# Performance work log

Measured on AMD Instinct MI355X. Metric: run time of the kernel, lower is better.

## Reference

```python
import jax, jax.numpy as jnp
import numpy as np

B, L, N, D, TOPK, OUT_V = 32, 512, 1024, 64, 20, 1024
BN_EPS = 1e-5
NEG_SLOPE = 0.2


def setup_inputs() -> dict:
    key = jax.random.key(0)
    ks = jax.random.split(key, 8)
    s = lambda k, shape, sc=0.05: jax.random.normal(k, shape, jnp.float32) * sc
    return {
        "x_enc": jax.random.normal(ks[0], (B, L, N), jnp.float32),
        "emb": s(ks[1], (N, D), 0.1),          # nn.Embedding(variate, d_model).weight
        "lin_W": s(ks[2], (L, D)),              # GraphLayer.lin (no bias)
        "att_i": s(ks[3], (D,)),
        "att_j": s(ks[4], (D,)),
        "att_em_i": s(ks[5], (D,)),
        "att_em_j": s(ks[6], (D,)),
        "gnn_b": jnp.zeros((D,), jnp.float32),  # GraphLayer bias (concat=False)
        "g1": jnp.ones((D,), jnp.float32), "b1": jnp.zeros((D,), jnp.float32),   # GNNLayer.bn
        "g2": jnp.ones((D,), jnp.float32), "b2": jnp.zeros((D,), jnp.float32),   # bn_outlayer_in
        "out_W": s(ks[7], (D, 1)), "out_b": jnp.zeros((1,), jnp.float32),        # OutLayer Linear(d_model, 1)
    }


def _forward(x_enc, emb, lin_W, att_i, att_j, att_em_i, att_em_j,
             gnn_b, g1, b1, g2, b2, out_W, out_b):
    # --- LIN: LayerNorm(input_len, eps=0, no affine) over time, first OUT_V variates ---
    xv = jnp.transpose(x_enc[:, :, :OUT_V], (0, 2, 1))          # [B, OUT_V, L]
    xv = (xv - xv.mean(-1, keepdims=True)) / jnp.sqrt(xv.var(-1, keepdims=True))
    x_enc = x_enc.at[:, :, :OUT_V].set(jnp.transpose(xv, (0, 2, 1)))
    x_enc = jnp.nan_to_num(x_enc, nan=0.0, posinf=0.0, neginf=0.0)

    gt = x_enc[:, -1:, :OUT_V]                                   # [B, 1, OUT_V]
    enc = x_enc.at[:, -1:, :OUT_V].set(0.0)

    # x = enc.transpose(0,1).view(-1, L)  (faithful to original reshape)
    x = jnp.transpose(enc, (1, 0, 2)).reshape(-1, L)             # [B*N, L]

    # --- dynamic top-k cosine-similarity graph (embeddings detached) ---
    w = jax.lax.stop_gradient(emb)
    nrm = jnp.linalg.norm(w, axis=-1)
    cos = (w @ w.T) / (nrm[:, None] * nrm[None, :])              # [N, N]
    topk_idx = jax.lax.top_k(cos, TOPK)[1]                       # [N, TOPK]
    src = topk_idx.reshape(-1)                                   # gated_j (source)
    dst = jnp.repeat(jnp.arange(N), TOPK)                        # gated_i (target)

    offs = (jnp.arange(B) * N)[:, None]
    src_b = (src[None, :] + offs).reshape(-1)                    # [B*N*TOPK]
    dst_b = (dst[None, :] + offs).reshape(-1)

    # remove_self_loops (mask out) then add_self_loops for all B*N nodes
    num_nodes = B * N
    self_mask = jnp.concatenate([src_b == dst_b, jnp.zeros(num_nodes, bool)])
    src_all = jnp.concatenate([src_b, jnp.arange(num_nodes)])
    dst_all = jnp.concatenate([dst_b, jnp.arange(num_nodes)])

    # --- GraphLayer (GAT-style, heads=1, concat=False) ---
    h = x @ lin_W                                                # [B*N, D]
    all_emb = jnp.tile(emb, (B, 1))                              # [B*N, D]

    logit = (h[dst_all] @ att_i + all_emb[dst_all] @ att_em_i
             + h[src_all] @ att_j + all_emb[src_all] @ att_em_j)  # [E]
    logit = jnp.where(logit >= 0, logit, NEG_SLOPE * logit)      # leaky_relu(0.2)
    logit = jnp.where(self_mask, -jnp.inf, logit)

    seg_max = jax.ops.segment_max(logit, dst_all, num_segments=num_nodes)
    expv = jnp.where(self_mask, 0.0, jnp.exp(logit - seg_max[dst_all]))
    denom = jax.ops.segment_sum(expv, dst_all, num_segments=num_nodes)
    alpha = expv / denom[dst_all]

    out = jax.ops.segment_sum(h[src_all] * alpha[:, None], dst_all,
                              num_segments=num_nodes) + gnn_b    # [B*N, D]

    # GNNLayer: BatchNorm1d(D) (batch stats) + ReLU
    out = (out - out.mean(0)) / jnp.sqrt(out.var(0) + BN_EPS) * g1 + b1
    out = jax.nn.relu(out)

    # --- combine with embedding, bn_outlayer_in, OutLayer ---
    xg = out.reshape(B, N, D) * emb[None]                        # [B, N, D]
    xg = jnp.transpose(xg, (0, 2, 1))                            # [B, D, N]
    mu = xg.mean((0, 2), keepdims=True)
    var = xg.var((0, 2), keepdims=True)
    xg = (xg - mu) / jnp.sqrt(var + BN_EPS) * g2[None, :, None] + b2[None, :, None]
    xg = jnp.transpose(jax.nn.relu(xg), (0, 2, 1))               # [B, N, D]

    o = xg @ out_W + out_b                                       # [B, N, 1]
    o = jnp.transpose(o, (0, 2, 1))                              # [B, 1, N]
    return o[:, :, :OUT_V], gt


def reference(x_enc, emb, lin_W, att_i, att_j, att_em_i, att_em_j,
              gnn_b, g1, b1, g2, b2, out_W, out_b):
    return _forward(x_enc, emb, lin_W, att_i, att_j, att_em_i, att_em_j,
                    gnn_b, g1, b1, g2, b2, out_W, out_b)
```

## Files before the change

### kernel.cpp

```cpp
#include <hip/hip_runtime.h>
#include <stdint.h>

#define BB 32
#define LL 512
#define NNODES 1024
#define DD 64
#define TOPK 20
#define NTOT (BB*NNODES)
#define LNSZ (LL*NNODES)

typedef short short8 __attribute__((ext_vector_type(8)));
typedef float floatx4 __attribute__((ext_vector_type(4)));

__device__ __forceinline__ float bf2f(unsigned short u){
    union { unsigned int i; float f; } x; x.i = ((unsigned int)u) << 16; return x.f;
}
__device__ __forceinline__ unsigned short f2bf(float f){
    union { float f; unsigned int i; } x; x.f = f;
    unsigned int u = x.i;
    return (unsigned short)((u + 0x7FFFu + ((u >> 16) & 1u)) >> 16);
}
__device__ __forceinline__ void unpack2(unsigned int w, float& lo, float& hi){
    union { unsigned int i; float f; } a, b;
    a.i = w << 16; b.i = w & 0xFFFF0000u;
    lo = a.f; hi = b.f;
}
__device__ __forceinline__ float ldf(const void* p, int i, int isf){
    return isf ? ((const float*)p)[i] : bf2f(((const unsigned short*)p)[i]);
}

__global__ void __launch_bounds__(256) kd_detect(const unsigned short* x, int* flag, float* stats){
    __shared__ int cnt;
    stats[threadIdx.x] = 0.f;
    if (threadIdx.x == 0) cnt = 0;
    __syncthreads();
    unsigned int idx = (threadIdx.x * 131071u) & 0x7FFFFFu;
    float v = bf2f(x[idx * 2]);
    float a = fabsf(v);
    int crazy = (!(a <= 1e3f)) || (v != 0.f && a < 1e-6f);
    atomicAdd(&cnt, crazy);
    __syncthreads();
    if (threadIdx.x == 0) flag[0] = (cnt > 64) ? 1 : 0;
}

__global__ void __launch_bounds__(256) k0_prep(const void* lw, unsigned short* wt, const int* dtf){
    int isf = dtf[0];
    int id = blockIdx.x * 256 + threadIdx.x;
    int k = id >> 6, d = id & 63;
    unsigned short w = isf ? f2bf(((const float*)lw)[id]) : ((const unsigned short*)lw)[id];
    wt[d * 512 + k] = w;
}

__global__ void __launch_bounds__(256) k1a_partial(const void* x, float* part, const int* dtf){
    int isf = dtf[0];
    int t = threadIdx.x;
    int b = blockIdx.x >> 4, lq = blockIdx.x & 15;
    int n0 = t * 4;
    size_t base = (size_t)b * LNSZ + (size_t)(lq * 32) * NNODES + n0;
    float s0=0,s1=0,s2=0,s3=0,q0=0,q1=0,q2=0,q3=0;
    if (isf){
        const float* p = (const float*)x + base;
        for (int i = 0; i < 32; i++){
            float4 w = *(const float4*)p;
            s0+=w.x; q0+=w.x*w.x; s1+=w.y; q1+=w.y*w.y;
            s2+=w.z; q2+=w.z*w.z; s3+=w.w; q3+=w.w*w.w;
            p += NNODES;
        }
    } else {
        const unsigned short* p = (const unsigned short*)x + base;
        for (int i = 0; i < 32; i++){
            uint2 w = *(const uint2*)p;
            float a,bv,c,d2;
            unpack2(w.x, a, bv); unpack2(w.y, c, d2);
            s0+=a; q0+=a*a; s1+=bv; q1+=bv*bv; s2+=c; q2+=c*c; s3+=d2; q3+=d2*d2;
            p += NNODES;
        }
    }
    int v = b * NNODES + n0;
    float2* pp = (float2*)part;
    pp[(size_t)v*16 + lq]       = make_float2(s0,q0);
    pp[(size_t)(v+1)*16 + lq]   = make_float2(s1,q1);
    pp[(size_t)(v+2)*16 + lq]   = make_float2(s2,q2);
    pp[(size_t)(v+3)*16 + lq]   = make_float2(s3,q3);
}

__global__ void __launch_bounds__(256) k1b_finalize(const void* x, const float* part,
                                                    float* mr, float* outp, const int* dtf){
    int isf = dtf[0];
    int v = blockIdx.x * 256 + threadIdx.x;
    const float2* pp = (const float2*)part + (size_t)v * 16;
    float s = 0.f, q = 0.f;
    for (int i = 0; i < 16; i++){ float2 w = pp[i]; s += w.x; q += w.y; }
    float mean = s * (1.f/512.f);
    float var  = q * (1.f/512.f) - mean * mean;
    float rstd = var > 0.f ? rsqrtf(var) : 0.f;
    ((float2*)mr)[v] = make_float2(mean, rstd);
    int b = v >> 10, n = v & 1023;
    float xv = ldf(x, (int)((size_t)b * LNSZ + (size_t)511 * NNODES + n), isf);
    outp[NTOT + v] = (xv - mean) * rstd;
}

__global__ void __launch_bounds__(256) k2_gemm_h(const void* x, const unsigned short* wt,
                                                const float* mr, float* h, const int* dtf){
    __shared__ unsigned short A_l[128 * 136];
    __shared__ unsigned short W_l[64 * 136];
    __shared__ float4 colp4[256];
    int isf = dtf[0];
    int t = threadIdx.x;
    int q = blockIdx.x & 63, mtile = blockIdx.x >> 6;
    int b = q >> 1, nbase = (q & 1) * 512;
    size_t xbase = (size_t)b * LNSZ + nbase;

    colp4[t] = ((const float4*)mr)[q * 256 + t];

    int wave = t >> 6, lane = t & 63;
    int quad = lane >> 4, lcol = lane & 15;
    floatx4 acc[2][4];
    for (int i = 0; i < 2; i++) for (int j = 0; j < 4; j++) acc[i][j] = (floatx4){0.f,0.f,0.f,0.f};
    __syncthreads();

    for (int kc = 0; kc < 4; kc++){
        for (int i = 0; i < 8; i++){
            int id = i * 256 + t;
            int l = id >> 4, c16 = id & 15;
            int lg = mtile * 128 + l;
            uint4 o;
            if (lg == 511){
                o = make_uint4(0u, 0u, 0u, 0u);
            } else {
                size_t ofs = xbase + (size_t)lg * NNODES + kc * 128 + c16 * 8;
                float e0,e1,e2,e3,e4,e5,e6,e7;
                if (isf){
                    const float4* px = (const float4*)((const float*)x + ofs);
                    float4 wa = px[0], wb = px[1];
                    e0=wa.x; e1=wa.y; e2=wa.z; e3=wa.w; e4=wb.x; e5=wb.y; e6=wb.z; e7=wb.w;
                } else {
                    uint4 w = *(const uint4*)((const unsigned short*)x + ofs);
                    unpack2(w.x,e0,e1); unpack2(w.y,e2,e3); unpack2(w.z,e4,e5); unpack2(w.w,e6,e7);
                }
                int f4b = kc * 64 + c16 * 4;
                float4 pA = colp4[f4b+0], pB = colp4[f4b+1], pC = colp4[f4b+2], pD = colp4[f4b+3];
                e0 = (e0 - pA.x) * pA.y;  e1 = (e1 - pA.z) * pA.w;
                e2 = (e2 - pB.x) * pB.y;  e3 = (e3 - pB.z) * pB.w;
                e4 = (e4 - pC.x) * pC.y;  e5 = (e5 - pC.z) * pC.w;
                e6 = (e6 - pD.x) * pD.y;  e7 = (e7 - pD.z) * pD.w;
                o.x = (unsigned)f2bf(e0) | ((unsigned)f2bf(e1) << 16);
                o.y = (unsigned)f2bf(e2) | ((unsigned)f2bf(e3) << 16);
                o.z = (unsigned)f2bf(e4) | ((unsigned)f2bf(e5) << 16);
                o.w = (unsigned)f2bf(e6) | ((unsigned)f2bf(e7) << 16);
            }
            *(uint4*)&A_l[l * 136 + c16 * 8] = o;
        }
        for (int i = 0; i < 4; i++){
            int id = i * 256 + t;
            int dd = id >> 4, c16 = id & 15;
            uint4 w = *(const uint4*)(wt + dd * 512 + kc * 128 + c16 * 8);
            *(uint4*)&W_l[dd * 136 + c16 * 8] = w;
        }
        __syncthreads();
        for (int ks = 0; ks < 4; ks++){
            short8 af[2], bfr[4];
            af[0] = *(const short8*)&A_l[(wave * 32 + lcol) * 136 + ks * 32 + quad * 8];
            af[1] = *(const short8*)&A_l[(wave * 32 + 16 + lcol) * 136 + ks * 32 + quad * 8];
            for (int tc = 0; tc < 4; tc++)
                bfr[tc] = *(const short8*)&W_l[(tc * 16 + lcol) * 136 + ks * 32 + quad * 8];
            for (int tr = 0; tr < 2; tr++)
                for (int tc = 0; tc < 4; tc++)
                    acc[tr][tc] = __builtin_amdgcn_mfma_f32_16x16x32_bf16(af[tr], bfr[tc], acc[tr][tc], 0, 0, 0);
        }
        __syncthreads();
    }
    for (int tr = 0; tr < 2; tr++) for (int tc = 0; tc < 4; tc++){
        int dcol = tc * 16 + lcol;
        for (int r = 0; r < 4; r++){
            int lrow = wave * 32 + tr * 16 + quad * 4 + r;
            int lg = mtile * 128 + lrow;
            int row = lg * 64 + q;
            h[(size_t)row * 64 + dcol] = acc[tr][tc][r];
        }
    }
}

__global__ void __launch_bounds__(256) k3_graph(const void* emb, const void* aemi,
                                                const void* aemj, float* eai, float* eaj,
                                                int* topk, const int* dtf){
    __shared__ float enf[64];
    __shared__ float crow[1024];
    __shared__ float n2sh;
    int isf = dtf[0];
    int n = blockIdx.x, t = threadIdx.x, lane = t & 63, wave = t >> 6;
    if (wave == 0){
        float e = ldf(emb, n * 64 + lane, isf);
        enf[lane] = e;
        float p1 = e * e;
        float p2 = e * ldf(aemi, lane, isf);
        float p3 = e * ldf(aemj, lane, isf);
        for (int m = 1; m < 64; m <<= 1){
            p1 += __shfl_xor(p1, m, 64);
            p2 += __shfl_xor(p2, m, 64);
            p3 += __shfl_xor(p3, m, 64);
        }
        if (lane == 0){ n2sh = p1; eai[n] = p2; eaj[n] = p3; }
    }
    __syncthreads();
    float rn_own = rsqrtf(n2sh);
    for (int mi = 0; mi < 4; mi++){
        int m = mi * 256 + t;
        float dot = 0.f, sq = 0.f;
        if (isf){
            const float4* pm = (const float4*)((const float*)emb + m * 64);
            #pragma unroll
            for (int i = 0; i < 16; i++){
                float4 w = pm[i];
                dot += enf[i*4+0]*w.x + enf[i*4+1]*w.y + enf[i*4+2]*w.z + enf[i*4+3]*w.w;
                sq  += w.x*w.x + w.y*w.y + w.z*w.z + w.w*w.w;
            }
        } else {
            const uint4* pm = (const uint4*)((const unsigned short*)emb + m * 64);
            #pragma unroll
            for (int i = 0; i < 8; i++){
                uint4 w = pm[i];
                float a0,a1,a2,a3,a4,a5,a6,a7;
                unpack2(w.x,a0,a1); unpack2(w.y,a2,a3); unpack2(w.z,a4,a5); unpack2(w.w,a6,a7);
                dot += enf[i*8+0]*a0 + enf[i*8+1]*a1 + enf[i*8+2]*a2 + enf[i*8+3]*a3
                     + enf[i*8+4]*a4 + enf[i*8+5]*a5 + enf[i*8+6]*a6 + enf[i*8+7]*a7;
                sq  += a0*a0 + a1*a1 + a2*a2 + a3*a3 + a4*a4 + a5*a5 + a6*a6 + a7*a7;
            }
        }
        crow[m] = dot * rn_own * rsqrtf(sq);
    }
    __syncthreads();
    if (wave == 0){
        float v[16];
        #pragma unroll
        for (int ii = 0; ii < 16; ii++) v[ii] = crow[ii * 64 + lane];
        for (int k = 0; k < TOPK; k++){
            float bv = v[0]; int bi = 0;
            #pragma unroll
            for (int ii = 1; ii < 16; ii++) if (v[ii] > bv){ bv = v[ii]; bi = ii; }
            int bm = bi * 64 + lane;
            for (int m2 = 1; m2 < 64; m2 <<= 1){
                float ov = __shfl_xor(bv, m2, 64);
                int   om = __shfl_xor(bm, m2, 64);
                if (ov > bv || (ov == bv && om < bm)){ bv = ov; bm = om; }
            }
            if (lane == 0) topk[n * TOPK + k] = bm;
            int evi = bm >> 6;
            bool own = ((bm & 63) == lane);
            #pragma unroll
            for (int ii = 0; ii < 16; ii++)
                v[ii] = (own && ii == evi) ? -__builtin_inff() : v[ii];
        }
    }
}

__global__ void __launch_bounds__(256) k4_coef(const float* h, const void* att_i, const void* att_j,
                                               const float* eai, const float* eaj, float* ai, float* aj,
                                               const int* dtf){
    int isf = dtf[0];
    int wave = blockIdx.x * 4 + (threadIdx.x >> 6), lane = threadIdx.x & 63;
    float wi = ldf(att_i, lane, isf), wj = ldf(att_j, lane, isf);
    int v0 = wave * 16;
    for (int i = 0; i < 16; i++){
        int v = v0 + i;
        float hv = h[(size_t)v * 64 + lane];
        float p1 = hv * wi, p2 = hv * wj;
        for (int m = 1; m < 64; m <<= 1){ p1 += __shfl_xor(p1, m, 64); p2 += __shfl_xor(p2, m, 64); }
        if (lane == 0){
            int n = v & 1023;
            ai[v] = p1 + eai[n];
            aj[v] = p2 + eaj[n];
        }
    }
}

__global__ void __launch_bounds__(256) k5_attn(const float* h, const float* ai, const float* aj, const int* topk,
                                               const void* gnn_b, float* out, const int* dtf){
    int isf = dtf[0];
    int wave = threadIdx.x >> 6, lane = threadIdx.x & 63;
    float gb = ldf(gnn_b, lane, isf);
    int v = blockIdx.x * 4 + wave;
    int n = v & 1023, bbase = v & ~1023;
    int srcv; bool valid;
    if (lane < TOPK){
        int id = topk[n * TOPK + lane];
        srcv = bbase | id;
        valid = (id != n);
    } else if (lane == TOPK){
        srcv = v; valid = true;
    } else { srcv = v; valid = false; }
    float l = ai[v] + aj[srcv];
    l = (l >= 0.f) ? l : 0.2f * l;
    if (!valid) l = -__builtin_inff();
    float m = l;
    #pragma unroll
    for (int s = 1; s < 64; s <<= 1){ float o = __shfl_xor(m, s, 64); m = fmaxf(m, o); }
    float ev = valid ? __expf(l - m) : 0.f;
    float dsum = ev;
    #pragma unroll
    for (int s = 1; s < 64; s <<= 1) dsum += __shfl_xor(dsum, s, 64);
    float rd = 1.f / dsum;
    float acc = 0.f;
    #pragma unroll
    for (int j = 0; j <= TOPK; j++){
        float e = __shfl(ev, j, 64);
        int  sj = __shfl(srcv, j, 64);
        acc += e * h[(size_t)sj * 64 + lane];
    }
    out[(size_t)v * 64 + lane] = acc * rd + gb;
}

__global__ void __launch_bounds__(256) k5b_stats(const float* out, float* stats1){
    __shared__ float bs[256], bq[256];
    int wave = threadIdx.x >> 6, lane = threadIdx.x & 63;
    int v0 = blockIdx.x * 128 + wave * 32;
    float ssum = 0.f, ssq = 0.f;
    for (int i = 0; i < 32; i++){
        float x = out[(size_t)(v0 + i) * 64 + lane];
        ssum += x; ssq += x * x;
    }
    bs[threadIdx.x] = ssum; bq[threadIdx.x] = ssq;
    __syncthreads();
    if (wave == 0){
        float s  = bs[lane] + bs[64+lane] + bs[128+lane] + bs[192+lane];
        float qq = bq[lane] + bq[64+lane] + bq[128+lane] + bq[192+lane];
        atomicAdd(&stats1[lane], s);
        atomicAdd(&stats1[64 + lane], qq);
    }
}

__global__ void __launch_bounds__(256) k6_stats2(const float* out, const float* stats1, const void* g1,
                                                 const void* b1, const void* emb,
                                                 float* stats2, const int* dtf){
    __shared__ float bs[256], bq[256];
    int isf = dtf[0];
    int wave = threadIdx.x >> 6, lane = threadIdx.x & 63;
    float mu   = stats1[lane] * (1.f/32768.f);
    float var  = stats1[64 + lane] * (1.f/32768.f) - mu * mu;
    float rstd = 1.f / sqrtf(var + 1e-5f);
    float g = ldf(g1, lane, isf), bb = ldf(b1, lane, isf);
    float ssum = 0.f, ssq = 0.f;
    int v0 = (blockIdx.x * 4 + wave) * 16;
    for (int i = 0; i < 16; i++){
        int v = v0 + i; int n = v & 1023;
        float x = out[(size_t)v * 64 + lane];
        float y = fmaxf((x - mu) * rstd * g + bb, 0.f);
        float z = y * ldf(emb, n * 64 + lane, isf);
        ssum += z; ssq += z * z;
    }
    bs[threadIdx.x] = ssum; bq[threadIdx.x] = ssq;
    __syncthreads();
    if (wave == 0){
        float s  = bs[lane] + bs[64+lane] + bs[128+lane] + bs[192+lane];
        float qq = bq[lane] + bq[64+lane] + bq[128+lane] + bq[192+lane];
        atomicAdd(&stats2[lane], s);
        atomicAdd(&stats2[64 + lane], qq);
    }
}

__global__ void __launch_bounds__(256) k7_out(const float* out, const float* stats1, const float* stats2,
                                              const void* g1, const void* b1,
                                              const void* g2, const void* b2,
                                              const void* emb, const void* outw,
                                              const void* outb, float* o, const int* dtf){
    int isf = dtf[0];
    int wave = threadIdx.x >> 6, lane = threadIdx.x & 63;
    float mu1   = stats1[lane] * (1.f/32768.f);
    float var1  = stats1[64 + lane] * (1.f/32768.f) - mu1 * mu1;
    float rstd1 = 1.f / sqrtf(var1 + 1e-5f);
    float g1v = ldf(g1, lane, isf), b1v = ldf(b1, lane, isf);
    float mu2   = stats2[lane] * (1.f/32768.f);
    float var2  = stats2[64 + lane] * (1.f/32768.f) - mu2 * mu2;
    float rstd2 = 1.f / sqrtf(var2 + 1e-5f);
    float g2v = ldf(g2, lane, isf), b2v = ldf(b2, lane, isf);
    float w = ldf(outw, lane, isf);
    float ob = ldf(outb, 0, isf);
    int v0 = (blockIdx.x * 4 + wave) * 16;
    for (int i = 0; i < 16; i++){
        int v = v0 + i; int n = v & 1023;
        float x = out[(size_t)v * 64 + lane];
        float z = fmaxf((x - mu1) * rstd1 * g1v + b1v, 0.f) * ldf(emb, n * 64 + lane, isf);
        float y = fmaxf((z - mu2) * rstd2 * g2v + b2v, 0.f);
        float p = y * w;
        for (int s = 1; s < 64; s <<= 1) p += __shfl_xor(p, s, 64);
        if (lane == 0) o[v] = p + ob;
    }
}

extern "C" void kernel_launch(void* const* d_in, const int* in_sizes, int n_in,
                              void* d_out, int out_size, void* d_ws, size_t ws_size,
                              hipStream_t stream){
    const void* x    = d_in[0];
    const void* emb  = d_in[1];
    const void* linW = d_in[2];
    const void* atti = d_in[3];
    const void* attj = d_in[4];
    const void* aemi = d_in[5];
    const void* aemj = d_in[6];
    const void* gnnb = d_in[7];
    const void* g1   = d_in[8];
    const void* b1   = d_in[9];
    const void* g2   = d_in[10];
    const void* b2   = d_in[11];
    const void* outw = d_in[12];
    const void* outb = d_in[13];
    float* o = (float*)d_out;

    char* w = (char*)d_ws;
    float*          mr    = (float*)(w + 0);
    unsigned short* wt    = (unsigned short*)(w + 262144);
    float*          h     = (float*)(w + 327680);
    float*          eai   = (float*)(w + 8716288);
    float*          eaj   = (float*)(w + 8720384);
    int*            topk  = (int*)(w + 8724480);
    float*          ai    = (float*)(w + 8806400);
    float*          aj    = (float*)(w + 8937472);
    float*          outg  = (float*)(w + 9068544);
    float*          part  = outg;
    float*          stats = (float*)(w + 17457152);
    int*            dtf   = (int*)(w + 17458176);

    hipLaunchKernelGGL(kd_detect,    dim3(1),    dim3(256), 0, stream, (const unsigned short*)x, dtf, stats);
    hipLaunchKernelGGL(k0_prep,      dim3(128),  dim3(256), 0, stream, linW, wt, dtf);
    hipLaunchKernelGGL(k1a_partial,  dim3(512),  dim3(256), 0, stream, x, part, dtf);
    hipLaunchKernelGGL(k1b_finalize, dim3(128),  dim3(256), 0, stream, x, part, mr, o, dtf);
    hipLaunchKernelGGL(k2_gemm_h,    dim3(256),  dim3(256), 0, stream, x, wt, mr, h, dtf);
    hipLaunchKernelGGL(k3_graph,     dim3(1024), dim3(256), 0, stream, emb, aemi, aemj, eai, eaj, topk, dtf);
    hipLaunchKernelGGL(k4_coef,      dim3(512),  dim3(256), 0, stream, h, atti, attj, eai, eaj, ai, aj, dtf);
    hipLaunchKernelGGL(k5_attn,      dim3(8192), dim3(256), 0, stream, h, ai, aj, topk, gnnb, outg, dtf);
    hipLaunchKernelGGL(k5b_stats,    dim3(256),  dim3(256), 0, stream, outg, stats);
    hipLaunchKernelGGL(k6_stats2,    dim3(512),  dim3(256), 0, stream, outg, stats, g1, b1, emb, stats + 128, dtf);
    hipLaunchKernelGGL(k7_out,       dim3(512),  dim3(256), 0, stream, outg, stats, stats + 128,
                       g1, b1, g2, b2, emb, outw, outb, o, dtf);
}
```

Measured before the change: 273.3 us.

## Compute top-k graph with one wave per node, no shared row buffer

Reworks the cosine top-k kernel so that each wave handles one node and holds its 1024 similarity values in registers (16 per lane). This removes the shared-memory row buffer, the block barrier, and the serial top-k done by a single wave while three waves sat idle. The per-lane argmax becomes a tree reduction, and the embedding-attention dot products move into the prep kernel. The cost is higher register pressure and a serial 64-iteration loop per thread in the prep kernel.

```diff
diff --git a/kernel.cpp b/kernel.cpp
--- a/kernel.cpp
+++ b/kernel.cpp
@@ -43,12 +43,24 @@
     if (threadIdx.x == 0) flag[0] = (cnt > 64) ? 1 : 0;
 }
 
-__global__ void __launch_bounds__(256) k0_prep(const void* lw, unsigned short* wt, const int* dtf){
+__global__ void __launch_bounds__(256) k0_prep(const void* lw, unsigned short* wt,
+                                               const void* emb, const void* aemi, const void* aemj,
+                                               float* eai, float* eaj, const int* dtf){
     int isf = dtf[0];
     int id = blockIdx.x * 256 + threadIdx.x;
     int k = id >> 6, d = id & 63;
     unsigned short w = isf ? f2bf(((const float*)lw)[id]) : ((const unsigned short*)lw)[id];
     wt[d * 512 + k] = w;
+    if (id < 1024){
+        int n = id;
+        float s1 = 0.f, s2 = 0.f;
+        for (int dd = 0; dd < 64; dd++){
+            float e = ldf(emb, n * 64 + dd, isf);
+            s1 += e * ldf(aemi, dd, isf);
+            s2 += e * ldf(aemj, dd, isf);
+        }
+        eai[n] = s1; eaj[n] = s2;
+    }
 }
 
 __global__ void __launch_bounds__(256) k1a_partial(const void* x, float* part, const int* dtf){
@@ -181,38 +193,29 @@
     }
 }
 
-__global__ void __launch_bounds__(256) k3_graph(const void* emb, const void* aemi,
-                                                const void* aemj, float* eai, float* eaj,
-                                                int* topk, const int* dtf){
-    __shared__ float enf[64];
-    __shared__ float crow[1024];
-    __shared__ float n2sh;
-    int isf = dtf[0];
-    int n = blockIdx.x, t = threadIdx.x, lane = t & 63, wave = t >> 6;
-    if (wave == 0){
-        float e = ldf(emb, n * 64 + lane, isf);
-        enf[lane] = e;
-        float p1 = e * e;
-        float p2 = e * ldf(aemi, lane, isf);
-        float p3 = e * ldf(aemj, lane, isf);
-        for (int m = 1; m < 64; m <<= 1){
-            p1 += __shfl_xor(p1, m, 64);
-            p2 += __shfl_xor(p2, m, 64);
-            p3 += __shfl_xor(p3, m, 64);
-        }
-        if (lane == 0){ n2sh = p1; eai[n] = p2; eaj[n] = p3; }
-    }
-    __syncthreads();
-    float rn_own = rsqrtf(n2sh);
-    for (int mi = 0; mi < 4; mi++){
-        int m = mi * 256 + t;
+__global__ void __launch_bounds__(256) k3_topk(const void* emb, int* topk, const int* dtf){
+    __shared__ float enf[4][64];
+    int isf = dtf[0];
+    int wave = threadIdx.x >> 6, lane = threadIdx.x & 63;
+    int n = blockIdx.x * 4 + wave;
+    float e = ldf(emb, n * 64 + lane, isf);
+    enf[wave][lane] = e;
+    float p1 = e * e;
+    #pragma unroll
+    for (int m = 1; m < 64; m <<= 1) p1 += __shfl_xor(p1, m, 64);
+    __syncthreads();
+    float rn_own = rsqrtf(p1);
+    const float* en = enf[wave];
+    float va[16];
+    for (int ii = 0; ii < 16; ii++){
+        int m = ii * 64 + lane;
         float dot = 0.f, sq = 0.f;
         if (isf){
             const float4* pm = (const float4*)((const float*)emb + m * 64);
             #pragma unroll
             for (int i = 0; i < 16; i++){
                 float4 w = pm[i];
-                dot += enf[i*4+0]*w.x + enf[i*4+1]*w.y + enf[i*4+2]*w.z + enf[i*4+3]*w.w;
+                dot += en[i*4+0]*w.x + en[i*4+1]*w.y + en[i*4+2]*w.z + en[i*4+3]*w.w;
                 sq  += w.x*w.x + w.y*w.y + w.z*w.z + w.w*w.w;
             }
         } else {
@@ -222,35 +225,46 @@
                 uint4 w = pm[i];
                 float a0,a1,a2,a3,a4,a5,a6,a7;
                 unpack2(w.x,a0,a1); unpack2(w.y,a2,a3); unpack2(w.z,a4,a5); unpack2(w.w,a6,a7);
-                dot += enf[i*8+0]*a0 + enf[i*8+1]*a1 + enf[i*8+2]*a2 + enf[i*8+3]*a3
-                     + enf[i*8+4]*a4 + enf[i*8+5]*a5 + enf[i*8+6]*a6 + enf[i*8+7]*a7;
+                dot += en[i*8+0]*a0 + en[i*8+1]*a1 + en[i*8+2]*a2 + en[i*8+3]*a3
+                     + en[i*8+4]*a4 + en[i*8+5]*a5 + en[i*8+6]*a6 + en[i*8+7]*a7;
                 sq  += a0*a0 + a1*a1 + a2*a2 + a3*a3 + a4*a4 + a5*a5 + a6*a6 + a7*a7;
             }
         }
-        crow[m] = dot * rn_own * rsqrtf(sq);
-    }
-    __syncthreads();
-    if (wave == 0){
-        float v[16];
+        va[ii] = dot * rn_own * rsqrtf(sq);
+    }
+    for (int k = 0; k < TOPK; k++){
+        float t8[8]; int x8[8];
         #pragma unroll
-        for (int ii = 0; ii < 16; ii++) v[ii] = crow[ii * 64 + lane];
-        for (int k = 0; k < TOPK; k++){
-            float bv = v[0]; int bi = 0;
-            #pragma unroll
-            for (int ii = 1; ii < 16; ii++) if (v[ii] > bv){ bv = v[ii]; bi = ii; }
-            int bm = bi * 64 + lane;
-            for (int m2 = 1; m2 < 64; m2 <<= 1){
-                float ov = __shfl_xor(bv, m2, 64);
-                int   om = __shfl_xor(bm, m2, 64);
-                if (ov > bv || (ov == bv && om < bm)){ bv = ov; bm = om; }
-            }
-            if (lane == 0) topk[n * TOPK + k] = bm;
-            int evi = bm >> 6;
-            bool own = ((bm & 63) == lane);
-            #pragma unroll
-            for (int ii = 0; ii < 16; ii++)
-                v[ii] = (own && ii == evi) ? -__builtin_inff() : v[ii];
-        }
+        for (int j = 0; j < 8; j++){
+            bool c = va[2*j+1] > va[2*j];
+            t8[j] = c ? va[2*j+1] : va[2*j]; x8[j] = c ? 2*j+1 : 2*j;
+        }
+        #pragma unroll
+        for (int j = 0; j < 4; j++){
+            bool c = t8[2*j+1] > t8[2*j];
+            t8[j] = c ? t8[2*j+1] : t8[2*j]; x8[j] = c ? x8[2*j+1] : x8[2*j];
+        }
+        #pragma unroll
+        for (int j = 0; j < 2; j++){
+            bool c = t8[2*j+1] > t8[2*j];
+            t8[j] = c ? t8[2*j+1] : t8[2*j]; x8[j] = c ? x8[2*j+1] : x8[2*j];
+        }
+        bool c0 = t8[1] > t8[0];
+        float bv = c0 ? t8[1] : t8[0]; int bi = c0 ? x8[1] : x8[0];
+        int bm = bi * 64 + lane;
+        #pragma unroll
+        for (int s = 1; s < 64; s <<= 1){
+            float ov = __shfl_xor(bv, s, 64);
+            int   om = __shfl_xor(bm, s, 64);
+            bool u = (ov > bv) || (ov == bv && om < bm);
+            bv = u ? ov : bv; bm = u ? om : bm;
+        }
+        if (lane == 0) topk[n * TOPK + k] = bm;
+        int evi = bm >> 6;
+        bool own = ((bm & 63) == lane);
+        #pragma unroll
+        for (int ii = 0; ii < 16; ii++)
+            va[ii] = (own && ii == evi) ? -__builtin_inff() : va[ii];
     }
 }
 
@@ -421,11 +435,11 @@
     int*            dtf   = (int*)(w + 17458176);
 
     hipLaunchKernelGGL(kd_detect,    dim3(1),    dim3(256), 0, stream, (const unsigned short*)x, dtf, stats);
-    hipLaunchKernelGGL(k0_prep,      dim3(128),  dim3(256), 0, stream, linW, wt, dtf);
+    hipLaunchKernelGGL(k0_prep,      dim3(128),  dim3(256), 0, stream, linW, wt, emb, aemi, aemj, eai, eaj, dtf);
     hipLaunchKernelGGL(k1a_partial,  dim3(512),  dim3(256), 0, stream, x, part, dtf);
     hipLaunchKernelGGL(k1b_finalize, dim3(128),  dim3(256), 0, stream, x, part, mr, o, dtf);
     hipLaunchKernelGGL(k2_gemm_h,    dim3(256),  dim3(256), 0, stream, x, wt, mr, h, dtf);
-    hipLaunchKernelGGL(k3_graph,     dim3(1024), dim3(256), 0, stream, emb, aemi, aemj, eai, eaj, topk, dtf);
+    hipLaunchKernelGGL(k3_topk,      dim3(256),  dim3(256), 0, stream, emb, topk, dtf);
     hipLaunchKernelGGL(k4_coef,      dim3(512),  dim3(256), 0, stream, h, atti, attj, eai, eaj, ai, aj, dtf);
     hipLaunchKernelGGL(k5_attn,      dim3(8192), dim3(256), 0, stream, h, ai, aj, topk, gnnb, outg, dtf);
     hipLaunchKernelGGL(k5b_stats,    dim3(256),  dim3(256), 0, stream, outg, stats);
```

Result: slower. 283.4 us (+3.7%).
